# Kernel tuning notes

Measured on AMD Instinct MI355X. Metric: run time of the kernel, lower is better.

Reference implementation:

```python
import jax, jax.numpy as jnp
import numpy as np

H = 1024   # hidden_size
NH = 32    # num_heads
D = H // NH  # head_dim = 32
M = 2      # num_timescales
BMIN, BMAX = 0.85, 0.9995
EPS = 1e-6
ROPE_BASE = 10000.0
LN_EPS = 1e-5


def setup_inputs() -> dict:
    key = jax.random.key(0)
    ks = jax.random.split(key, 8)
    b, t = 4, 1024
    x = jax.random.normal(ks[0], (b, t, H), jnp.float32)
    # xavier-uniform for q/k/v/out (matches _reset_parameters)
    sc = (6.0 / (H + H)) ** 0.5
    Wq = jax.random.uniform(ks[1], (H, H), jnp.float32, -sc, sc)
    Wk = jax.random.uniform(ks[2], (H, H), jnp.float32, -sc, sc)
    Wv = jax.random.uniform(ks[3], (H, H), jnp.float32, -sc, sc)
    Wout = jax.random.uniform(ks[4], (H, H), jnp.float32, -sc, sc)
    bout = jnp.zeros((H,), jnp.float32)
    # beta_proj: random weight, bias set so sigmoid(bias) = linspace(beta_min, beta_max)
    scb = (6.0 / (H + NH * M)) ** 0.5
    Wbeta = jax.random.uniform(ks[5], (NH * M, H), jnp.float32, -scb, scb)
    targets = jnp.linspace(BMIN, BMAX, M)
    bbeta = jnp.tile(jnp.log(targets / (1.0 - targets)), NH)  # repeat 'm -> (h m)'
    # mix_proj initialized to zeros (uniform mixing via softmax)
    Wmix = jnp.zeros((NH * M, H), jnp.float32)
    bmix = jnp.zeros((NH * M,), jnp.float32)
    ln_g = jnp.ones((H,), jnp.float32)
    ln_b = jnp.zeros((H,), jnp.float32)
    return dict(x=x, Wq=Wq, Wk=Wk, Wv=Wv, Wbeta=Wbeta, bbeta=bbeta,
                Wmix=Wmix, bmix=bmix, Wout=Wout, bout=bout, ln_g=ln_g, ln_b=ln_b)


def _rope(u, cos, sin):
    # u: [b,t,h,d] with d even; cos/sin: [1,t,1,d//2]
    half = D // 2
    u1, u2 = u[..., :half], u[..., half:]
    return jnp.concatenate([u1 * cos - u2 * sin, u1 * sin + u2 * cos], axis=-1)


def _forward(x, Wq, Wk, Wv, Wbeta, bbeta, Wmix, bmix, Wout, bout, ln_g, ln_b):
    b, t, _ = x.shape
    q = (x @ Wq.T).reshape(b, t, NH, D)
    k = (x @ Wk.T).reshape(b, t, NH, D)
    v = (x @ Wv.T).reshape(b, t, NH, D)
    # RoPE cache
    half = D // 2
    inv_freq = 1.0 / (ROPE_BASE ** (jnp.arange(half, dtype=jnp.float32) / half))
    freqs = jnp.arange(t, dtype=jnp.float32)[:, None] * inv_freq  # [t,half]
    cos = jnp.cos(freqs)[None, :, None, :]
    sin = jnp.sin(freqs)[None, :, None, :]
    q = _rope(q, cos, sin)
    k = _rope(k, cos, sin)
    phi_q = jax.nn.elu(q) + 1.0
    phi_k = jax.nn.elu(k) + 1.0
    beta = jnp.clip(jax.nn.sigmoid((x @ Wbeta.T + bbeta).reshape(b, t, NH, M)), BMIN, BMAX)
    mix = jax.nn.softmax((x @ Wmix.T + bmix).reshape(b, t, NH, M), axis=-1)

    def step(carry, xs):
        S, K = carry  # S:[b,h,M,d,d]  K:[b,h,M,d]
        pq, pk, vt, bt, mt = xs  # [b,h,d],[b,h,d],[b,h,d],[b,h,M],[b,h,M]
        K = K * bt[..., None] + pk[:, :, None, :]
        S = S * bt[..., None, None] + pk[:, :, None, :, None] * vt[:, :, None, None, :]
        num = jnp.einsum('bhd,bhmdc->bhmc', pq, S)
        den = jnp.einsum('bhd,bhmd->bhm', pq, K) + EPS
        y = jnp.sum(num / den[..., None] * mt[..., None], axis=2)  # [b,h,d]
        return (S, K), y

    S0 = jnp.zeros((b, NH, M, D, D), x.dtype)
    K0 = jnp.zeros((b, NH, M, D), x.dtype)
    tf = lambda a: jnp.moveaxis(a, 1, 0)  # time-major for scan
    _, ys = jax.lax.scan(step, (S0, K0), (tf(phi_q), tf(phi_k), tf(v), tf(beta), tf(mix)))
    y = jnp.moveaxis(ys, 0, 1).reshape(b, t, H) @ Wout.T + bout
    z = x + y  # residual; dropout is identity in eval
    mu = z.mean(-1, keepdims=True)
    var = ((z - mu) ** 2).mean(-1, keepdims=True)
    return (z - mu) / jnp.sqrt(var + LN_EPS) * ln_g + ln_b


def reference(x, Wq, Wk, Wv, Wbeta, bbeta, Wmix, bmix, Wout, bout, ln_g, ln_b):
    return _forward(x, Wq, Wk, Wv, Wbeta, bbeta, Wmix, bmix, Wout, bout, ln_g, ln_b)
```

## Files before the change

kernel.cpp:

```cpp
#include <hip/hip_runtime.h>
#include <math.h>

#define TT 1024
#define BB 4
#define HH 1024
#define NHH 32
#define CL 64
#define NCH (TT/CL)

typedef unsigned short u16;
typedef __attribute__((ext_vector_type(8))) short short8;
typedef __attribute__((ext_vector_type(8))) unsigned short u16x8;
typedef __attribute__((ext_vector_type(4))) float floatx4;

__device__ __forceinline__ float sigmoidf_(float x){ return 1.f/(1.f+expf(-x)); }
__device__ __forceinline__ u16 f2b(float f){
  union { float f; unsigned u; } x; x.f = f;
  unsigned r = x.u + 0x7FFFu + ((x.u >> 16) & 1u);
  return (u16)(r >> 16);
}
__device__ __forceinline__ float b2f(u16 v){
  union { unsigned u; float f; } x; x.u = ((unsigned)v) << 16;
  return x.f;
}

__global__ __launch_bounds__(256) void cast_all_k(
    const float* __restrict__ x, const float* __restrict__ Wq, const float* __restrict__ Wk,
    const float* __restrict__ Wv, const float* __restrict__ Wbeta, const float* __restrict__ Wmix,
    const float* __restrict__ Wout,
    u16* __restrict__ x_bf, u16* __restrict__ Wf, u16* __restrict__ Wout_bf,
    float* __restrict__ ct, float* __restrict__ st)
{
  int gid = blockIdx.x*256 + threadIdx.x;
  if (gid < 16384) {
    int t = gid >> 4, j = gid & 15;
    float invf = powf(10000.f, -(float)j/16.f);
    float ang = (float)t * invf;
    ct[gid] = cosf(ang);
    st[gid] = sinf(ang);
  }
  size_t e = (size_t)gid*4;
  const float* src; u16* dst; size_t so, dof;
  if      (e < 4194304) { src=x;     dst=x_bf;    so=e;          dof=so; }
  else if (e < 5242880) { src=Wq;    dst=Wf;      so=e-4194304;  dof=so; }
  else if (e < 6291456) { src=Wk;    dst=Wf;      so=e-5242880;  dof=so+1048576; }
  else if (e < 7340032) { src=Wv;    dst=Wf;      so=e-6291456;  dof=so+2097152; }
  else if (e < 7405568) { src=Wbeta; dst=Wf;      so=e-7340032;  dof=so+3145728; }
  else if (e < 7471104) { src=Wmix;  dst=Wf;      so=e-7405568;  dof=so+3211264; }
  else                  { src=Wout;  dst=Wout_bf; so=e-7471104;  dof=so; }
  float4 f = *reinterpret_cast<const float4*>(src + so);
  ushort4 u; u.x=f2b(f.x); u.y=f2b(f.y); u.z=f2b(f.z); u.w=f2b(f.w);
  *reinterpret_cast<ushort4*>(dst + dof) = u;
}

__global__ __launch_bounds__(256) void gemm_qkv_k(
    const u16* __restrict__ A, const u16* __restrict__ W,
    const float* __restrict__ ct, const float* __restrict__ st,
    u16* __restrict__ qkv, float* __restrict__ bmraw)
{
  __shared__ u16 As[128*64];
  __shared__ u16 Ws[128*64];
  const int tid = threadIdx.x;
  const int lane = tid & 63;
  const int wave = tid >> 6;
  const int wm = wave >> 1, wn = wave & 1;
  const int bx = blockIdx.x;
  const int row0 = blockIdx.y*128, col0 = bx*128;
  const int lr = lane & 15, lkg = lane >> 4;

  floatx4 acc[4][4];
  #pragma unroll
  for (int mt=0; mt<4; ++mt)
    #pragma unroll
    for (int nt=0; nt<4; ++nt)
      acc[mt][nt] = (floatx4){0.f,0.f,0.f,0.f};

  for (int k0 = 0; k0 < 1024; k0 += 64) {
    __syncthreads();
    #pragma unroll
    for (int it = 0; it < 4; ++it) {
      int li  = it*256 + tid;
      int row = li >> 3, ckp = li & 7;
      int ck  = ckp ^ (row & 7);
      const u16* ga = A + (size_t)(row0+row)*1024 + k0 + ck*8;
      const u16* gw = W + (size_t)(col0+row)*1024 + k0 + ck*8;
      __builtin_amdgcn_global_load_lds(
          (const __attribute__((address_space(1))) void*)ga,
          (__attribute__((address_space(3))) void*)(As + (size_t)(li & ~63)*8), 16, 0, 0);
      __builtin_amdgcn_global_load_lds(
          (const __attribute__((address_space(1))) void*)gw,
          (__attribute__((address_space(3))) void*)(Ws + (size_t)(li & ~63)*8), 16, 0, 0);
    }
    __syncthreads();
    #pragma unroll
    for (int kk = 0; kk < 64; kk += 32) {
      short8 af[4], wf[4];
      const int ckw = (kk >> 3) + lkg;
      #pragma unroll
      for (int t = 0; t < 4; ++t) {
        int rowA = wm*64 + t*16 + lr;
        int rowW = wn*64 + t*16 + lr;
        af[t] = *reinterpret_cast<const short8*>(As + rowA*64 + (ckw ^ (rowA & 7))*8);
        wf[t] = *reinterpret_cast<const short8*>(Ws + rowW*64 + (ckw ^ (rowW & 7))*8);
      }
      #pragma unroll
      for (int mt = 0; mt < 4; ++mt)
        #pragma unroll
        for (int nt = 0; nt < 4; ++nt)
          acc[mt][nt] = __builtin_amdgcn_mfma_f32_16x16x32_bf16(af[mt], wf[nt], acc[mt][nt], 0, 0, 0);
    }
  }
  if (bx < 16) {
    #pragma unroll
    for (int mt = 0; mt < 4; ++mt) {
      #pragma unroll
      for (int r = 0; r < 4; ++r) {
        int row = row0 + wm*64 + mt*16 + lkg*4 + r;
        int t = row & (TT-1);
        float c_ = ct[t*16 + lr], s_ = st[t*16 + lr];
        #pragma unroll
        for (int nt = 0; nt < 4; nt += 2) {
          float u1 = acc[mt][nt][r], u2 = acc[mt][nt+1][r];
          float r1 = u1*c_ - u2*s_;
          float r2 = u1*s_ + u2*c_;
          r1 = r1 > 0.f ? r1+1.f : expf(r1);
          r2 = r2 > 0.f ? r2+1.f : expf(r2);
          int col = col0 + wn*64 + nt*16 + lr;
          qkv[(size_t)row*3072 + col]      = f2b(r1);
          qkv[(size_t)row*3072 + col + 16] = f2b(r2);
        }
      }
    }
  } else if (bx < 24) {
    #pragma unroll
    for (int mt = 0; mt < 4; ++mt)
      #pragma unroll
      for (int r = 0; r < 4; ++r) {
        int row = row0 + wm*64 + mt*16 + lkg*4 + r;
        #pragma unroll
        for (int nt = 0; nt < 4; ++nt) {
          int col = col0 + wn*64 + nt*16 + lr;
          qkv[(size_t)row*3072 + col] = f2b(acc[mt][nt][r]);
        }
      }
  } else {
    #pragma unroll
    for (int mt = 0; mt < 4; ++mt)
      #pragma unroll
      for (int r = 0; r < 4; ++r) {
        int row = row0 + wm*64 + mt*16 + lkg*4 + r;
        #pragma unroll
        for (int nt = 0; nt < 4; ++nt) {
          int col = col0 + wn*64 + nt*16 + lr - 3072;
          bmraw[(size_t)row*128 + col] = acc[mt][nt][r];
        }
      }
  }
}

__global__ __launch_bounds__(256) void gemm_out_k(
    const u16* __restrict__ A, const u16* __restrict__ W,
    const float* __restrict__ xr, const float* __restrict__ bout,
    float* __restrict__ Z)
{
  __shared__ u16 As[128*64];
  __shared__ u16 Ws[64*64];
  const int tid = threadIdx.x;
  const int lane = tid & 63;
  const int wave = tid >> 6;
  const int row0 = blockIdx.y*128, col0 = blockIdx.x*64;
  const int lr = lane & 15, lkg = lane >> 4;
  floatx4 acc[2][4];
  #pragma unroll
  for (int mt=0; mt<2; ++mt)
    #pragma unroll
    for (int nt=0; nt<4; ++nt)
      acc[mt][nt] = (floatx4){0.f,0.f,0.f,0.f};
  for (int k0 = 0; k0 < 1024; k0 += 64) {
    __syncthreads();
    #pragma unroll
    for (int it = 0; it < 4; ++it) {
      int li  = it*256 + tid;
      int row = li >> 3, ckp = li & 7;
      int ck  = ckp ^ (row & 7);
      const u16* ga = A + (size_t)(row0+row)*1024 + k0 + ck*8;
      __builtin_amdgcn_global_load_lds(
          (const __attribute__((address_space(1))) void*)ga,
          (__attribute__((address_space(3))) void*)(As + (size_t)(li & ~63)*8), 16, 0, 0);
    }
    #pragma unroll
    for (int it = 0; it < 2; ++it) {
      int li  = it*256 + tid;
      int row = li >> 3, ckp = li & 7;
      int ck  = ckp ^ (row & 7);
      const u16* gw = W + (size_t)(col0+row)*1024 + k0 + ck*8;
      __builtin_amdgcn_global_load_lds(
          (const __attribute__((address_space(1))) void*)gw,
          (__attribute__((address_space(3))) void*)(Ws + (size_t)(li & ~63)*8), 16, 0, 0);
    }
    __syncthreads();
    #pragma unroll
    for (int kk = 0; kk < 64; kk += 32) {
      short8 af[2], wf[4];
      const int ckw = (kk >> 3) + lkg;
      #pragma unroll
      for (int t = 0; t < 2; ++t) {
        int rowA = wave*32 + t*16 + lr;
        af[t] = *reinterpret_cast<const short8*>(As + rowA*64 + (ckw ^ (rowA & 7))*8);
      }
      #pragma unroll
      for (int t = 0; t < 4; ++t) {
        int rowW = t*16 + lr;
        wf[t] = *reinterpret_cast<const short8*>(Ws + rowW*64 + (ckw ^ (rowW & 7))*8);
      }
      #pragma unroll
      for (int mt = 0; mt < 2; ++mt)
        #pragma unroll
        for (int nt = 0; nt < 4; ++nt)
          acc[mt][nt] = __builtin_amdgcn_mfma_f32_16x16x32_bf16(af[mt], wf[nt], acc[mt][nt], 0, 0, 0);
    }
  }
  #pragma unroll
  for (int mt = 0; mt < 2; ++mt)
    #pragma unroll
    for (int r = 0; r < 4; ++r) {
      int row = row0 + wave*32 + mt*16 + lkg*4 + r;
      #pragma unroll
      for (int nt = 0; nt < 4; ++nt) {
        int col = col0 + nt*16 + lr;
        Z[(size_t)row*HH + col] = acc[mt][nt][r] + bout[col] + xr[(size_t)row*HH + col];
      }
    }
}

__global__ __launch_bounds__(256) void scan_delta_k(
    const u16* __restrict__ qkv, const float* __restrict__ bmraw,
    const float* __restrict__ bbeta,
    float* __restrict__ dS, float* __restrict__ dK,
    float* __restrict__ pLg, float* __restrict__ pg)
{
  __shared__ __align__(16) u16 K2T[2][32][72];
  __shared__ __align__(16) u16 VT[32][72];
  __shared__ float bets[2][64], pbuf[2][64], wjs[2][64], pLs[2];
  const int ch = blockIdx.x, h = blockIdx.y, b = blockIdx.z;
  const int bh = b*NHH + h;
  const int tid = threadIdx.x;
  const int t0 = ch*CL;
  const int j = tid >> 2, oct = tid & 3;
  size_t rowbase = (size_t)(b*TT + t0 + j)*3072 + h*32 + oct*8;
  u16x8 k8 = *reinterpret_cast<const u16x8*>(qkv + rowbase + 1024);
  u16x8 v8 = *reinterpret_cast<const u16x8*>(qkv + rowbase + 2048);
  if (tid < 128) {
    int m = tid & 1, tl = tid >> 1;
    float bv = bmraw[(size_t)(b*TT + t0 + tl)*128 + h*2 + m] + bbeta[h*2 + m];
    bets[m][tl] = fminf(fmaxf(sigmoidf_(bv), 0.85f), 0.9995f);
  }
  #pragma unroll
  for (int dd = 0; dd < 8; ++dd) VT[oct*8+dd][j] = v8[dd];
  __syncthreads();
  if (tid < 128) {
    int m = tid >> 6, l = tid & 63;
    float p = bets[m][l];
    #pragma unroll
    for (int off = 1; off < 64; off <<= 1) {
      float o = __shfl_up(p, off);
      if (l >= off) p *= o;
    }
    pbuf[m][l] = p;
    if (l == 63) pLs[m] = p;
  }
  __syncthreads();
  if (tid < 128) {
    int m = tid >> 6, l = tid & 63;
    wjs[m][l] = pLs[m] / pbuf[m][l];
    pg[(((size_t)bh*NCH + ch)*2 + m)*64 + l] = pbuf[m][l];
  }
  if (tid < 2) pLg[((size_t)bh*NCH + ch)*2 + tid] = pLs[tid];
  __syncthreads();
  float w0 = wjs[0][j], w1 = wjs[1][j];
  #pragma unroll
  for (int dd = 0; dd < 8; ++dd) {
    float kv = b2f(k8[dd]);
    K2T[0][oct*8+dd][j] = f2b(kv*w0);
    K2T[1][oct*8+dd][j] = f2b(kv*w1);
  }
  __syncthreads();
  {
    const int wv = tid >> 6, lane = tid & 63, lr = lane & 15, kg = lane >> 4;
    const int m = wv >> 1, mt = wv & 1;
    floatx4 a0 = (floatx4){0.f,0.f,0.f,0.f}, a1 = (floatx4){0.f,0.f,0.f,0.f};
    #pragma unroll
    for (int ks = 0; ks < 2; ++ks) {
      short8 af = *reinterpret_cast<const short8*>(&K2T[m][mt*16 + lr][ks*32 + kg*8]);
      short8 b0 = *reinterpret_cast<const short8*>(&VT[lr][ks*32 + kg*8]);
      short8 b1 = *reinterpret_cast<const short8*>(&VT[16 + lr][ks*32 + kg*8]);
      a0 = __builtin_amdgcn_mfma_f32_16x16x32_bf16(af, b0, a0, 0, 0, 0);
      a1 = __builtin_amdgcn_mfma_f32_16x16x32_bf16(af, b1, a1, 0, 0, 0);
    }
    size_t base = (((size_t)bh*NCH + ch)*2 + m)*1024;
    #pragma unroll
    for (int r = 0; r < 4; ++r) {
      int d = mt*16 + kg*4 + r;
      dS[base + d*32 + lr]      = a0[r];
      dS[base + d*32 + 16 + lr] = a1[r];
    }
  }
  if (tid < 64) {
    int m = tid >> 5, d = tid & 31;
    float s = 0.f;
    #pragma unroll
    for (int g = 0; g < 8; ++g) {
      u16x8 kk = *reinterpret_cast<const u16x8*>(&K2T[m][d][g*8]);
      #pragma unroll
      for (int dd = 0; dd < 8; ++dd) s += b2f(kk[dd]);
    }
    dK[(((size_t)bh*NCH + ch)*2 + m)*32 + d] = s;
  }
}

__global__ __launch_bounds__(256) void scan_state_k(
    float* dSS0, float* dKK0, const float* __restrict__ pLg)
{
  const int bhm = blockIdx.x >> 2, part = blockIdx.x & 3;
  const int bh = bhm >> 1, m = bhm & 1;
  const int idx = part*256 + threadIdx.x;
  float pls[NCH], dv[NCH];
  #pragma unroll
  for (int ch = 0; ch < NCH; ++ch) pls[ch] = pLg[((size_t)bh*NCH + ch)*2 + m];
  #pragma unroll
  for (int ch = 0; ch < NCH; ++ch) dv[ch] = dSS0[(((size_t)bh*NCH + ch)*2 + m)*1024 + idx];
  float S = 0.f;
  #pragma unroll
  for (int ch = 0; ch < NCH; ++ch) {
    dSS0[(((size_t)bh*NCH + ch)*2 + m)*1024 + idx] = S;
    S = fmaf(pls[ch], S, dv[ch]);
  }
  if (part == 0 && threadIdx.x < 32) {
    int d = threadIdx.x;
    float kv[NCH];
    #pragma unroll
    for (int ch = 0; ch < NCH; ++ch) kv[ch] = dKK0[(((size_t)bh*NCH + ch)*2 + m)*32 + d];
    float K0 = 0.f;
    #pragma unroll
    for (int ch = 0; ch < NCH; ++ch) {
      dKK0[(((size_t)bh*NCH + ch)*2 + m)*32 + d] = K0;
      K0 = fmaf(pls[ch], K0, kv[ch]);
    }
  }
}

__global__ __launch_bounds__(256) void scan_apply_k(
    const u16* __restrict__ qkv, const float* __restrict__ bmraw,
    const float* __restrict__ bmix,
    const float* __restrict__ S0g, const float* __restrict__ K0g,
    const float* __restrict__ pg, u16* __restrict__ yb)
{
  __shared__ __align__(16) u16 Qs[64][32], Ks[64][32];
  __shared__ __align__(16) u16 VT[32][72];
  __shared__ __align__(16) u16 At[2][64][72];
  __shared__ __align__(16) u16 S0T[2][2][32][40];
  __shared__ float K0s[2][32];
  __shared__ float pbv[2][64], ipb[2][64], mixs[2][64], coef[2][64];
  const int ch = blockIdx.x, h = blockIdx.y, b = blockIdx.z;
  const int bh = b*NHH + h;
  const int tid = threadIdx.x;
  const int t0 = ch*CL;
  {
    int j = tid >> 2, oct = tid & 3;
    size_t rb = (size_t)(b*TT + t0 + j)*3072 + h*32 + oct*8;
    u16x8 q8 = *reinterpret_cast<const u16x8*>(qkv + rb);
    u16x8 k8 = *reinterpret_cast<const u16x8*>(qkv + rb + 1024);
    u16x8 v8 = *reinterpret_cast<const u16x8*>(qkv + rb + 2048);
    *reinterpret_cast<u16x8*>(&Qs[j][oct*8]) = q8;
    *reinterpret_cast<u16x8*>(&Ks[j][oct*8]) = k8;
    #pragma unroll
    for (int dd = 0; dd < 8; ++dd) VT[oct*8+dd][j] = v8[dd];
  }
  for (int u = tid; u < 2048; u += 256) {
    int m = u >> 10, r = u & 1023, d = r >> 5, c = r & 31;
    float val = S0g[(((size_t)bh*NCH + ch)*2 + m)*1024 + r];
    u16 hv = f2b(val);
    float lo = val - b2f(hv);
    S0T[m][0][c][d] = hv;
    S0T[m][1][c][d] = f2b(lo);
  }
  if (tid < 64) {
    int m = tid >> 5, d = tid & 31;
    K0s[m][d] = K0g[(((size_t)bh*NCH + ch)*2 + m)*32 + d];
  }
  if (tid < 128) {
    int m = tid & 1, i = tid >> 1;
    float p = pg[(((size_t)bh*NCH + ch)*2 + m)*64 + i];
    pbv[m][i] = p;
    ipb[m][i] = 1.f/p;
  } else if (tid < 192) {
    int i = tid - 128;
    size_t rb = (size_t)(b*TT + t0 + i)*128 + 64 + h*2;
    float a0 = bmraw[rb]   + bmix[h*2];
    float a1 = bmraw[rb+1] + bmix[h*2+1];
    float mx = fmaxf(a0, a1);
    float e0 = expf(a0-mx), e1 = expf(a1-mx);
    float inv = 1.f/(e0+e1);
    mixs[0][i] = e0*inv; mixs[1][i] = e1*inv;
  }
  __syncthreads();
  {
    const int wv = tid >> 6, lane = tid & 63, lr = lane & 15, kg = lane >> 4;
    short8 aq = *reinterpret_cast<const short8*>(&Qs[wv*16 + lr][kg*8]);
    #pragma unroll
    for (int nt = 0; nt < 4; ++nt) {
      short8 bk = *reinterpret_cast<const short8*>(&Ks[nt*16 + lr][kg*8]);
      floatx4 a0 = (floatx4){0.f,0.f,0.f,0.f};
      a0 = __builtin_amdgcn_mfma_f32_16x16x32_bf16(aq, bk, a0, 0, 0, 0);
      int jg = nt*16 + lr;
      float ip0 = ipb[0][jg], ip1 = ipb[1][jg];
      #pragma unroll
      for (int r = 0; r < 4; ++r) {
        int ig = wv*16 + kg*4 + r;
        float val = a0[r];
        bool ok = (jg <= ig);
        At[0][ig][jg] = f2b(ok ? val*ip0 : 0.f);
        At[1][ig][jg] = f2b(ok ? val*ip1 : 0.f);
      }
    }
  }
  __syncthreads();
  if (tid < 128) {
    int m = tid & 1, i = tid >> 1;
    float qK0 = 0.f;
    #pragma unroll
    for (int g = 0; g < 4; ++g) {
      u16x8 qq = *reinterpret_cast<const u16x8*>(&Qs[i][g*8]);
      #pragma unroll
      for (int dd = 0; dd < 8; ++dd) qK0 = fmaf(b2f(qq[dd]), K0s[m][g*8+dd], qK0);
    }
    float As_ = 0.f;
    #pragma unroll
    for (int g = 0; g < 8; ++g) {
      u16x8 aa = *reinterpret_cast<const u16x8*>(&At[m][i][g*8]);
      #pragma unroll
      for (int dd = 0; dd < 8; ++dd) As_ += b2f(aa[dd]);
    }
    float den = pbv[m][i]*(qK0 + As_) + 1e-6f;
    coef[m][i] = mixs[m][i]*pbv[m][i]/den;
  }
  __syncthreads();
  {
    const int wv = tid >> 6, lane = tid & 63, lr = lane & 15, kg = lane >> 4;
    const int i0 = wv*16;
    floatx4 accY[2][2];
    #pragma unroll
    for (int m = 0; m < 2; ++m)
      #pragma unroll
      for (int nt = 0; nt < 2; ++nt)
        accY[m][nt] = (floatx4){0.f,0.f,0.f,0.f};
    short8 aq = *reinterpret_cast<const short8*>(&Qs[i0 + lr][kg*8]);
    #pragma unroll
    for (int m = 0; m < 2; ++m)
      #pragma unroll
      for (int nt = 0; nt < 2; ++nt) {
        short8 bhi = *reinterpret_cast<const short8*>(&S0T[m][0][nt*16 + lr][kg*8]);
        short8 blo = *reinterpret_cast<const short8*>(&S0T[m][1][nt*16 + lr][kg*8]);
        accY[m][nt] = __builtin_amdgcn_mfma_f32_16x16x32_bf16(aq, bhi, accY[m][nt], 0, 0, 0);
        accY[m][nt] = __builtin_amdgcn_mfma_f32_16x16x32_bf16(aq, blo, accY[m][nt], 0, 0, 0);
      }
    #pragma unroll
    for (int ks = 0; ks < 2; ++ks) {
      short8 a0f = *reinterpret_cast<const short8*>(&At[0][i0 + lr][ks*32 + kg*8]);
      short8 a1f = *reinterpret_cast<const short8*>(&At[1][i0 + lr][ks*32 + kg*8]);
      short8 b0 = *reinterpret_cast<const short8*>(&VT[lr][ks*32 + kg*8]);
      short8 b1 = *reinterpret_cast<const short8*>(&VT[16 + lr][ks*32 + kg*8]);
      accY[0][0] = __builtin_amdgcn_mfma_f32_16x16x32_bf16(a0f, b0, accY[0][0], 0, 0, 0);
      accY[0][1] = __builtin_amdgcn_mfma_f32_16x16x32_bf16(a0f, b1, accY[0][1], 0, 0, 0);
      accY[1][0] = __builtin_amdgcn_mfma_f32_16x16x32_bf16(a1f, b0, accY[1][0], 0, 0, 0);
      accY[1][1] = __builtin_amdgcn_mfma_f32_16x16x32_bf16(a1f, b1, accY[1][1], 0, 0, 0);
    }
    #pragma unroll
    for (int r = 0; r < 4; ++r) {
      int i = i0 + kg*4 + r;
      float c0 = coef[0][i], c1 = coef[1][i];
      size_t ob = (size_t)(b*TT + t0 + i)*HH + h*32;
      yb[ob + lr]      = f2b(c0*accY[0][0][r] + c1*accY[1][0][r]);
      yb[ob + 16 + lr] = f2b(c0*accY[0][1][r] + c1*accY[1][1][r]);
    }
  }
}

__global__ __launch_bounds__(256) void ln_k(
    const float* __restrict__ z, const float* __restrict__ g,
    const float* __restrict__ bta, float* __restrict__ out)
{
  const int row = blockIdx.x;
  const int tid = threadIdx.x;
  size_t o = (size_t)row*HH/4 + tid;
  float4 zv = reinterpret_cast<const float4*>(z)[o];
  float sum = zv.x+zv.y+zv.z+zv.w;
  float sq  = zv.x*zv.x + zv.y*zv.y + zv.z*zv.z + zv.w*zv.w;
  #pragma unroll
  for (int off=1; off<64; off<<=1){ sum += __shfl_xor(sum, off); sq += __shfl_xor(sq, off); }
  __shared__ float s1[4], s2[4];
  int w = tid>>6;
  if ((tid&63)==0){ s1[w]=sum; s2[w]=sq; }
  __syncthreads();
  sum = s1[0]+s1[1]+s1[2]+s1[3];
  sq  = s2[0]+s2[1]+s2[2]+s2[3];
  float mu  = sum * (1.f/1024.f);
  float var = sq * (1.f/1024.f) - mu*mu;
  float rstd = rsqrtf(var + 1e-5f);
  float4 gv = reinterpret_cast<const float4*>(g)[tid];
  float4 bv = reinterpret_cast<const float4*>(bta)[tid];
  float4 ov;
  ov.x = (zv.x-mu)*rstd*gv.x + bv.x;
  ov.y = (zv.y-mu)*rstd*gv.y + bv.y;
  ov.z = (zv.z-mu)*rstd*gv.z + bv.z;
  ov.w = (zv.w-mu)*rstd*gv.w + bv.w;
  reinterpret_cast<float4*>(out)[o] = ov;
}

extern "C" void kernel_launch(void* const* d_in, const int* in_sizes, int n_in,
                              void* d_out, int out_size, void* d_ws, size_t ws_size,
                              hipStream_t stream)
{
  const float* x     = (const float*)d_in[0];
  const float* Wq    = (const float*)d_in[1];
  const float* Wk    = (const float*)d_in[2];
  const float* Wv    = (const float*)d_in[3];
  const float* Wbeta = (const float*)d_in[4];
  const float* bbeta = (const float*)d_in[5];
  const float* Wmix  = (const float*)d_in[6];
  const float* bmix  = (const float*)d_in[7];
  const float* Wout  = (const float*)d_in[8];
  const float* bout  = (const float*)d_in[9];
  const float* ln_g  = (const float*)d_in[10];
  const float* ln_b  = (const float*)d_in[11];
  float* out = (float*)d_out;

  float* ws = (float*)d_ws;
  float* ct      = ws;
  float* st      = ws + 16384;
  u16*   x_bf    = (u16*)(ws + 32768);
  u16*   Wf      = (u16*)(ws + 2129920);
  u16*   Wout_bf = (u16*)(ws + 3768320);
  u16*   qkv     = (u16*)(ws + 4292608);
  float* bmraw   = ws + 10584064;
  float* dSS0    = ws + 11108352;
  float* dKK0    = ws + 15302656;
  float* pLg     = ws + 15433728;
  float* pg      = ws + 15437824;
  u16*   y_bf    = x_bf;
  float* z       = dSS0;

  cast_all_k<<<8320, 256, 0, stream>>>(x, Wq, Wk, Wv, Wbeta, Wmix, Wout,
                                       x_bf, Wf, Wout_bf, ct, st);
  gemm_qkv_k<<<dim3(25, 32), 256, 0, stream>>>(x_bf, Wf, ct, st, qkv, bmraw);
  dim3 gscan(NCH, 32, 4);
  scan_delta_k<<<gscan, 256, 0, stream>>>(qkv, bmraw, bbeta, dSS0, dKK0, pLg, pg);
  scan_state_k<<<1024, 256, 0, stream>>>(dSS0, dKK0, pLg);
  scan_apply_k<<<gscan, 256, 0, stream>>>(qkv, bmraw, bmix, dSS0, dKK0, pg, y_bf);
  gemm_out_k<<<dim3(16, 32), 256, 0, stream>>>(y_bf, Wout_bf, x, bout, z);
  ln_k<<<4096, 256, 0, stream>>>(z, ln_g, ln_b, out);
}
```

Baseline: 210.2 us.

## Fuse chunked scan into one sequential-chunk kernel with on-chip state

Replaces the three-kernel chunked scan (per-chunk deltas, cross-chunk state prefix, apply) with a single kernel. Each block owns one (batch, head, half of value dims) and walks all chunks sequentially, keeping the running S and K state in shared memory and prefetching the next chunk's q/k/v and gate inputs into registers. This removes the global round trips for dS/dK/pLg/pg and two launches. In exchange the grid shrinks to 256 blocks that each run a 16-step serial loop, so parallelism drops, and the QK^T and K-side work is duplicated across the two value halves.

```diff
diff --git a/kernel.cpp b/kernel.cpp
--- a/kernel.cpp
+++ b/kernel.cpp
@@ -233,255 +233,210 @@
     }
 }
 
-__global__ __launch_bounds__(256) void scan_delta_k(
+__global__ __launch_bounds__(256) void scan_fused_k(
     const u16* __restrict__ qkv, const float* __restrict__ bmraw,
-    const float* __restrict__ bbeta,
-    float* __restrict__ dS, float* __restrict__ dK,
-    float* __restrict__ pLg, float* __restrict__ pg)
+    const float* __restrict__ bbeta, const float* __restrict__ bmix,
+    u16* __restrict__ yb)
 {
+  __shared__ __align__(16) u16 Qs[64][40], Ks[64][40];
+  __shared__ __align__(16) u16 VT[16][72];
   __shared__ __align__(16) u16 K2T[2][32][72];
-  __shared__ __align__(16) u16 VT[32][72];
-  __shared__ float bets[2][64], pbuf[2][64], wjs[2][64], pLs[2];
-  const int ch = blockIdx.x, h = blockIdx.y, b = blockIdx.z;
-  const int bh = b*NHH + h;
+  __shared__ __align__(16) u16 At[2][64][72];
+  __shared__ __align__(16) u16 S0T[2][2][16][40];
+  __shared__ float Ss[2][32][17];
+  __shared__ float K0s[2][32];
+  __shared__ float bets[2][64], pbv[2][64], ipb[2][64], wjs[2][64], mixs[2][64], coef[2][64];
+  __shared__ float pLs[2];
+
+  const int chalf = blockIdx.x, h = blockIdx.y, b = blockIdx.z;
   const int tid = threadIdx.x;
-  const int t0 = ch*CL;
-  const int j = tid >> 2, oct = tid & 3;
-  size_t rowbase = (size_t)(b*TT + t0 + j)*3072 + h*32 + oct*8;
-  u16x8 k8 = *reinterpret_cast<const u16x8*>(qkv + rowbase + 1024);
-  u16x8 v8 = *reinterpret_cast<const u16x8*>(qkv + rowbase + 2048);
-  if (tid < 128) {
-    int m = tid & 1, tl = tid >> 1;
-    float bv = bmraw[(size_t)(b*TT + t0 + tl)*128 + h*2 + m] + bbeta[h*2 + m];
-    bets[m][tl] = fminf(fmaxf(sigmoidf_(bv), 0.85f), 0.9995f);
+  const int lane = tid & 63, wv = tid >> 6;
+  const int lr = lane & 15, kg = lane >> 4;
+  const int jrow = tid >> 2, oct = tid & 3;
+
+  for (int u = tid; u < 2*32*17; u += 256) ((float*)Ss)[u] = 0.f;
+  if (tid < 64) K0s[tid>>5][tid&31] = 0.f;
+
+  const float bb  = (tid < 128) ? bbeta[h*2 + (tid&1)] : 0.f;
+  const float bm0 = bmix[h*2], bm1 = bmix[h*2+1];
+
+  u16x8 q8, k8; ushort4 v4; float bmv = 0.f, mr0 = 0.f, mr1 = 0.f;
+  {
+    size_t rb = (size_t)(b*TT + jrow)*3072 + h*32;
+    q8 = *reinterpret_cast<const u16x8*>(qkv + rb + oct*8);
+    k8 = *reinterpret_cast<const u16x8*>(qkv + rb + 1024 + oct*8);
+    v4 = *reinterpret_cast<const ushort4*>(qkv + rb + 2048 + chalf*16 + oct*4);
+    if (tid < 128) bmv = bmraw[(size_t)(b*TT + (tid>>1))*128 + h*2 + (tid&1)];
+    else if (tid < 192) {
+      int i = tid - 128;
+      size_t mb = (size_t)(b*TT + i)*128 + 64 + h*2;
+      mr0 = bmraw[mb]; mr1 = bmraw[mb+1];
+    }
   }
-  #pragma unroll
-  for (int dd = 0; dd < 8; ++dd) VT[oct*8+dd][j] = v8[dd];
-  __syncthreads();
-  if (tid < 128) {
-    int m = tid >> 6, l = tid & 63;
-    float p = bets[m][l];
-    #pragma unroll
-    for (int off = 1; off < 64; off <<= 1) {
-      float o = __shfl_up(p, off);
-      if (l >= off) p *= o;
-    }
-    pbuf[m][l] = p;
-    if (l == 63) pLs[m] = p;
-  }
-  __syncthreads();
-  if (tid < 128) {
-    int m = tid >> 6, l = tid & 63;
-    wjs[m][l] = pLs[m] / pbuf[m][l];
-    pg[(((size_t)bh*NCH + ch)*2 + m)*64 + l] = pbuf[m][l];
-  }
-  if (tid < 2) pLg[((size_t)bh*NCH + ch)*2 + tid] = pLs[tid];
-  __syncthreads();
-  float w0 = wjs[0][j], w1 = wjs[1][j];
-  #pragma unroll
-  for (int dd = 0; dd < 8; ++dd) {
-    float kv = b2f(k8[dd]);
-    K2T[0][oct*8+dd][j] = f2b(kv*w0);
-    K2T[1][oct*8+dd][j] = f2b(kv*w1);
-  }
-  __syncthreads();
-  {
-    const int wv = tid >> 6, lane = tid & 63, lr = lane & 15, kg = lane >> 4;
-    const int m = wv >> 1, mt = wv & 1;
-    floatx4 a0 = (floatx4){0.f,0.f,0.f,0.f}, a1 = (floatx4){0.f,0.f,0.f,0.f};
-    #pragma unroll
-    for (int ks = 0; ks < 2; ++ks) {
-      short8 af = *reinterpret_cast<const short8*>(&K2T[m][mt*16 + lr][ks*32 + kg*8]);
-      short8 b0 = *reinterpret_cast<const short8*>(&VT[lr][ks*32 + kg*8]);
-      short8 b1 = *reinterpret_cast<const short8*>(&VT[16 + lr][ks*32 + kg*8]);
-      a0 = __builtin_amdgcn_mfma_f32_16x16x32_bf16(af, b0, a0, 0, 0, 0);
-      a1 = __builtin_amdgcn_mfma_f32_16x16x32_bf16(af, b1, a1, 0, 0, 0);
-    }
-    size_t base = (((size_t)bh*NCH + ch)*2 + m)*1024;
-    #pragma unroll
-    for (int r = 0; r < 4; ++r) {
-      int d = mt*16 + kg*4 + r;
-      dS[base + d*32 + lr]      = a0[r];
-      dS[base + d*32 + 16 + lr] = a1[r];
-    }
-  }
-  if (tid < 64) {
-    int m = tid >> 5, d = tid & 31;
-    float s = 0.f;
-    #pragma unroll
-    for (int g = 0; g < 8; ++g) {
-      u16x8 kk = *reinterpret_cast<const u16x8*>(&K2T[m][d][g*8]);
-      #pragma unroll
-      for (int dd = 0; dd < 8; ++dd) s += b2f(kk[dd]);
-    }
-    dK[(((size_t)bh*NCH + ch)*2 + m)*32 + d] = s;
-  }
-}
-
-__global__ __launch_bounds__(256) void scan_state_k(
-    float* dSS0, float* dKK0, const float* __restrict__ pLg)
-{
-  const int bhm = blockIdx.x >> 2, part = blockIdx.x & 3;
-  const int bh = bhm >> 1, m = bhm & 1;
-  const int idx = part*256 + threadIdx.x;
-  float pls[NCH], dv[NCH];
-  #pragma unroll
-  for (int ch = 0; ch < NCH; ++ch) pls[ch] = pLg[((size_t)bh*NCH + ch)*2 + m];
-  #pragma unroll
-  for (int ch = 0; ch < NCH; ++ch) dv[ch] = dSS0[(((size_t)bh*NCH + ch)*2 + m)*1024 + idx];
-  float S = 0.f;
-  #pragma unroll
+
   for (int ch = 0; ch < NCH; ++ch) {
-    dSS0[(((size_t)bh*NCH + ch)*2 + m)*1024 + idx] = S;
-    S = fmaf(pls[ch], S, dv[ch]);
-  }
-  if (part == 0 && threadIdx.x < 32) {
-    int d = threadIdx.x;
-    float kv[NCH];
-    #pragma unroll
-    for (int ch = 0; ch < NCH; ++ch) kv[ch] = dKK0[(((size_t)bh*NCH + ch)*2 + m)*32 + d];
-    float K0 = 0.f;
-    #pragma unroll
-    for (int ch = 0; ch < NCH; ++ch) {
-      dKK0[(((size_t)bh*NCH + ch)*2 + m)*32 + d] = K0;
-      K0 = fmaf(pls[ch], K0, kv[ch]);
-    }
-  }
-}
-
-__global__ __launch_bounds__(256) void scan_apply_k(
-    const u16* __restrict__ qkv, const float* __restrict__ bmraw,
-    const float* __restrict__ bmix,
-    const float* __restrict__ S0g, const float* __restrict__ K0g,
-    const float* __restrict__ pg, u16* __restrict__ yb)
-{
-  __shared__ __align__(16) u16 Qs[64][32], Ks[64][32];
-  __shared__ __align__(16) u16 VT[32][72];
-  __shared__ __align__(16) u16 At[2][64][72];
-  __shared__ __align__(16) u16 S0T[2][2][32][40];
-  __shared__ float K0s[2][32];
-  __shared__ float pbv[2][64], ipb[2][64], mixs[2][64], coef[2][64];
-  const int ch = blockIdx.x, h = blockIdx.y, b = blockIdx.z;
-  const int bh = b*NHH + h;
-  const int tid = threadIdx.x;
-  const int t0 = ch*CL;
-  {
-    int j = tid >> 2, oct = tid & 3;
-    size_t rb = (size_t)(b*TT + t0 + j)*3072 + h*32 + oct*8;
-    u16x8 q8 = *reinterpret_cast<const u16x8*>(qkv + rb);
-    u16x8 k8 = *reinterpret_cast<const u16x8*>(qkv + rb + 1024);
-    u16x8 v8 = *reinterpret_cast<const u16x8*>(qkv + rb + 2048);
-    *reinterpret_cast<u16x8*>(&Qs[j][oct*8]) = q8;
-    *reinterpret_cast<u16x8*>(&Ks[j][oct*8]) = k8;
-    #pragma unroll
-    for (int dd = 0; dd < 8; ++dd) VT[oct*8+dd][j] = v8[dd];
-  }
-  for (int u = tid; u < 2048; u += 256) {
-    int m = u >> 10, r = u & 1023, d = r >> 5, c = r & 31;
-    float val = S0g[(((size_t)bh*NCH + ch)*2 + m)*1024 + r];
-    u16 hv = f2b(val);
-    float lo = val - b2f(hv);
-    S0T[m][0][c][d] = hv;
-    S0T[m][1][c][d] = f2b(lo);
-  }
-  if (tid < 64) {
-    int m = tid >> 5, d = tid & 31;
-    K0s[m][d] = K0g[(((size_t)bh*NCH + ch)*2 + m)*32 + d];
-  }
-  if (tid < 128) {
-    int m = tid & 1, i = tid >> 1;
-    float p = pg[(((size_t)bh*NCH + ch)*2 + m)*64 + i];
-    pbv[m][i] = p;
-    ipb[m][i] = 1.f/p;
-  } else if (tid < 192) {
-    int i = tid - 128;
-    size_t rb = (size_t)(b*TT + t0 + i)*128 + 64 + h*2;
-    float a0 = bmraw[rb]   + bmix[h*2];
-    float a1 = bmraw[rb+1] + bmix[h*2+1];
-    float mx = fmaxf(a0, a1);
-    float e0 = expf(a0-mx), e1 = expf(a1-mx);
-    float inv = 1.f/(e0+e1);
-    mixs[0][i] = e0*inv; mixs[1][i] = e1*inv;
-  }
-  __syncthreads();
-  {
-    const int wv = tid >> 6, lane = tid & 63, lr = lane & 15, kg = lane >> 4;
-    short8 aq = *reinterpret_cast<const short8*>(&Qs[wv*16 + lr][kg*8]);
+    const int t0 = ch*CL;
+    __syncthreads();
+    *reinterpret_cast<u16x8*>(&Qs[jrow][oct*8]) = q8;
+    *reinterpret_cast<u16x8*>(&Ks[jrow][oct*8]) = k8;
+    u16x8 k8c = k8;
+    {
+      const u16* vp = reinterpret_cast<const u16*>(&v4);
+      #pragma unroll
+      for (int u2 = 0; u2 < 4; ++u2) VT[oct*4+u2][jrow] = vp[u2];
+    }
+    float mr0c = mr0, mr1c = mr1;
+    if (tid < 128) bets[tid&1][tid>>1] = fminf(fmaxf(sigmoidf_(bmv + bb), 0.85f), 0.9995f);
+    if (ch < NCH-1) {
+      int t0n = t0 + CL;
+      size_t rb = (size_t)(b*TT + t0n + jrow)*3072 + h*32;
+      q8 = *reinterpret_cast<const u16x8*>(qkv + rb + oct*8);
+      k8 = *reinterpret_cast<const u16x8*>(qkv + rb + 1024 + oct*8);
+      v4 = *reinterpret_cast<const ushort4*>(qkv + rb + 2048 + chalf*16 + oct*4);
+      if (tid < 128) bmv = bmraw[(size_t)(b*TT + t0n + (tid>>1))*128 + h*2 + (tid&1)];
+      else if (tid < 192) {
+        int i = tid - 128;
+        size_t mb = (size_t)(b*TT + t0n + i)*128 + 64 + h*2;
+        mr0 = bmraw[mb]; mr1 = bmraw[mb+1];
+      }
+    }
+    __syncthreads();
+    if (tid < 128) {
+      float p = bets[wv][lane];
+      #pragma unroll
+      for (int off = 1; off < 64; off <<= 1) {
+        float o = __shfl_up(p, off);
+        if (lane >= off) p *= o;
+      }
+      float pl = __shfl(p, 63);
+      pbv[wv][lane] = p;
+      ipb[wv][lane] = 1.f/p;
+      wjs[wv][lane] = pl/p;
+      if (lane == 63) pLs[wv] = p;
+    } else if (tid < 192) {
+      int i = tid - 128;
+      float a0v = mr0c + bm0, a1v = mr1c + bm1;
+      float mx = fmaxf(a0v, a1v);
+      float e0 = expf(a0v-mx), e1 = expf(a1v-mx);
+      float inv = 1.f/(e0+e1);
+      mixs[0][i] = e0*inv; mixs[1][i] = e1*inv;
+    }
+    floatx4 a0r[4];
+    {
+      short8 aq = *reinterpret_cast<const short8*>(&Qs[wv*16 + lr][kg*8]);
+      #pragma unroll
+      for (int nt = 0; nt < 4; ++nt) {
+        short8 bk = *reinterpret_cast<const short8*>(&Ks[nt*16 + lr][kg*8]);
+        a0r[nt] = (floatx4){0.f,0.f,0.f,0.f};
+        a0r[nt] = __builtin_amdgcn_mfma_f32_16x16x32_bf16(aq, bk, a0r[nt], 0, 0, 0);
+      }
+    }
+    #pragma unroll
+    for (int i2 = 0; i2 < 4; ++i2) {
+      int e = tid*4 + i2;
+      int m = e >> 9, rem = e & 511, c = rem >> 5, d = rem & 31;
+      float val = Ss[m][d][c];
+      u16 hv = f2b(val);
+      S0T[m][0][c][d] = hv;
+      S0T[m][1][c][d] = f2b(val - b2f(hv));
+    }
+    __syncthreads();
     #pragma unroll
     for (int nt = 0; nt < 4; ++nt) {
-      short8 bk = *reinterpret_cast<const short8*>(&Ks[nt*16 + lr][kg*8]);
-      floatx4 a0 = (floatx4){0.f,0.f,0.f,0.f};
-      a0 = __builtin_amdgcn_mfma_f32_16x16x32_bf16(aq, bk, a0, 0, 0, 0);
       int jg = nt*16 + lr;
       float ip0 = ipb[0][jg], ip1 = ipb[1][jg];
       #pragma unroll
       for (int r = 0; r < 4; ++r) {
         int ig = wv*16 + kg*4 + r;
-        float val = a0[r];
+        float val = a0r[nt][r];
         bool ok = (jg <= ig);
         At[0][ig][jg] = f2b(ok ? val*ip0 : 0.f);
         At[1][ig][jg] = f2b(ok ? val*ip1 : 0.f);
       }
     }
-  }
-  __syncthreads();
-  if (tid < 128) {
-    int m = tid & 1, i = tid >> 1;
-    float qK0 = 0.f;
-    #pragma unroll
-    for (int g = 0; g < 4; ++g) {
-      u16x8 qq = *reinterpret_cast<const u16x8*>(&Qs[i][g*8]);
-      #pragma unroll
-      for (int dd = 0; dd < 8; ++dd) qK0 = fmaf(b2f(qq[dd]), K0s[m][g*8+dd], qK0);
-    }
-    float As_ = 0.f;
-    #pragma unroll
-    for (int g = 0; g < 8; ++g) {
-      u16x8 aa = *reinterpret_cast<const u16x8*>(&At[m][i][g*8]);
-      #pragma unroll
-      for (int dd = 0; dd < 8; ++dd) As_ += b2f(aa[dd]);
-    }
-    float den = pbv[m][i]*(qK0 + As_) + 1e-6f;
-    coef[m][i] = mixs[m][i]*pbv[m][i]/den;
-  }
-  __syncthreads();
-  {
-    const int wv = tid >> 6, lane = tid & 63, lr = lane & 15, kg = lane >> 4;
-    const int i0 = wv*16;
-    floatx4 accY[2][2];
-    #pragma unroll
-    for (int m = 0; m < 2; ++m)
-      #pragma unroll
-      for (int nt = 0; nt < 2; ++nt)
-        accY[m][nt] = (floatx4){0.f,0.f,0.f,0.f};
-    short8 aq = *reinterpret_cast<const short8*>(&Qs[i0 + lr][kg*8]);
-    #pragma unroll
-    for (int m = 0; m < 2; ++m)
-      #pragma unroll
-      for (int nt = 0; nt < 2; ++nt) {
-        short8 bhi = *reinterpret_cast<const short8*>(&S0T[m][0][nt*16 + lr][kg*8]);
-        short8 blo = *reinterpret_cast<const short8*>(&S0T[m][1][nt*16 + lr][kg*8]);
-        accY[m][nt] = __builtin_amdgcn_mfma_f32_16x16x32_bf16(aq, bhi, accY[m][nt], 0, 0, 0);
-        accY[m][nt] = __builtin_amdgcn_mfma_f32_16x16x32_bf16(aq, blo, accY[m][nt], 0, 0, 0);
-      }
-    #pragma unroll
-    for (int ks = 0; ks < 2; ++ks) {
-      short8 a0f = *reinterpret_cast<const short8*>(&At[0][i0 + lr][ks*32 + kg*8]);
-      short8 a1f = *reinterpret_cast<const short8*>(&At[1][i0 + lr][ks*32 + kg*8]);
-      short8 b0 = *reinterpret_cast<const short8*>(&VT[lr][ks*32 + kg*8]);
-      short8 b1 = *reinterpret_cast<const short8*>(&VT[16 + lr][ks*32 + kg*8]);
-      accY[0][0] = __builtin_amdgcn_mfma_f32_16x16x32_bf16(a0f, b0, accY[0][0], 0, 0, 0);
-      accY[0][1] = __builtin_amdgcn_mfma_f32_16x16x32_bf16(a0f, b1, accY[0][1], 0, 0, 0);
-      accY[1][0] = __builtin_amdgcn_mfma_f32_16x16x32_bf16(a1f, b0, accY[1][0], 0, 0, 0);
-      accY[1][1] = __builtin_amdgcn_mfma_f32_16x16x32_bf16(a1f, b1, accY[1][1], 0, 0, 0);
-    }
-    #pragma unroll
-    for (int r = 0; r < 4; ++r) {
-      int i = i0 + kg*4 + r;
-      float c0 = coef[0][i], c1 = coef[1][i];
-      size_t ob = (size_t)(b*TT + t0 + i)*HH + h*32;
-      yb[ob + lr]      = f2b(c0*accY[0][0][r] + c1*accY[1][0][r]);
-      yb[ob + 16 + lr] = f2b(c0*accY[0][1][r] + c1*accY[1][1][r]);
+    {
+      float w0 = wjs[0][jrow], w1 = wjs[1][jrow];
+      #pragma unroll
+      for (int dd = 0; dd < 8; ++dd) {
+        float kv = b2f(k8c[dd]);
+        K2T[0][oct*8+dd][jrow] = f2b(kv*w0);
+        K2T[1][oct*8+dd][jrow] = f2b(kv*w1);
+      }
+    }
+    __syncthreads();
+    if (tid < 128) {
+      int m = tid & 1, i = tid >> 1;
+      float qK0 = 0.f;
+      #pragma unroll
+      for (int g = 0; g < 4; ++g) {
+        u16x8 qq = *reinterpret_cast<const u16x8*>(&Qs[i][g*8]);
+        #pragma unroll
+        for (int dd = 0; dd < 8; ++dd) qK0 = fmaf(b2f(qq[dd]), K0s[m][g*8+dd], qK0);
+      }
+      float As_ = 0.f;
+      #pragma unroll
+      for (int g = 0; g < 8; ++g) {
+        u16x8 aa = *reinterpret_cast<const u16x8*>(&At[m][i][g*8]);
+        #pragma unroll
+        for (int dd = 0; dd < 8; ++dd) As_ += b2f(aa[dd]);
+      }
+      float den = pbv[m][i]*(qK0 + As_) + 1e-6f;
+      coef[m][i] = mixs[m][i]*pbv[m][i]/den;
+    } else {
+      int m = wv - 2;
+      float pl = pLs[m];
+      #pragma unroll
+      for (int dt = 0; dt < 2; ++dt) {
+        floatx4 acc = (floatx4){0.f,0.f,0.f,0.f};
+        #pragma unroll
+        for (int ks = 0; ks < 2; ++ks) {
+          short8 af = *reinterpret_cast<const short8*>(&K2T[m][dt*16 + lr][ks*32 + kg*8]);
+          short8 bv = *reinterpret_cast<const short8*>(&VT[lr][ks*32 + kg*8]);
+          acc = __builtin_amdgcn_mfma_f32_16x16x32_bf16(af, bv, acc, 0, 0, 0);
+        }
+        #pragma unroll
+        for (int r = 0; r < 4; ++r) {
+          int d = dt*16 + kg*4 + r;
+          Ss[m][d][lr] = fmaf(pl, Ss[m][d][lr], acc[r]);
+        }
+      }
+    }
+    __syncthreads();
+    {
+      floatx4 accY[2];
+      short8 aq = *reinterpret_cast<const short8*>(&Qs[wv*16 + lr][kg*8]);
+      #pragma unroll
+      for (int m = 0; m < 2; ++m) {
+        accY[m] = (floatx4){0.f,0.f,0.f,0.f};
+        short8 bhi = *reinterpret_cast<const short8*>(&S0T[m][0][lr][kg*8]);
+        short8 blo = *reinterpret_cast<const short8*>(&S0T[m][1][lr][kg*8]);
+        accY[m] = __builtin_amdgcn_mfma_f32_16x16x32_bf16(aq, bhi, accY[m], 0, 0, 0);
+        accY[m] = __builtin_amdgcn_mfma_f32_16x16x32_bf16(aq, blo, accY[m], 0, 0, 0);
+        #pragma unroll
+        for (int ks = 0; ks < 2; ++ks) {
+          short8 af = *reinterpret_cast<const short8*>(&At[m][wv*16 + lr][ks*32 + kg*8]);
+          short8 bv = *reinterpret_cast<const short8*>(&VT[lr][ks*32 + kg*8]);
+          accY[m] = __builtin_amdgcn_mfma_f32_16x16x32_bf16(af, bv, accY[m], 0, 0, 0);
+        }
+      }
+      #pragma unroll
+      for (int r = 0; r < 4; ++r) {
+        int i = wv*16 + kg*4 + r;
+        float c0 = coef[0][i], c1 = coef[1][i];
+        yb[(size_t)(b*TT + t0 + i)*HH + h*32 + chalf*16 + lr]
+            = f2b(c0*accY[0][r] + c1*accY[1][r]);
+      }
+    }
+    if (tid < 64) {
+      int m = tid >> 5, d = tid & 31;
+      float s = 0.f;
+      #pragma unroll
+      for (int g = 0; g < 8; ++g) {
+        u16x8 kk = *reinterpret_cast<const u16x8*>(&K2T[m][d][g*8]);
+        #pragma unroll
+        for (int dd = 0; dd < 8; ++dd) s += b2f(kk[dd]);
+      }
+      K0s[m][d] = fmaf(pLs[m], K0s[m][d], s);
     }
   }
 }
@@ -543,20 +498,13 @@
   u16*   Wout_bf = (u16*)(ws + 3768320);
   u16*   qkv     = (u16*)(ws + 4292608);
   float* bmraw   = ws + 10584064;
-  float* dSS0    = ws + 11108352;
-  float* dKK0    = ws + 15302656;
-  float* pLg     = ws + 15433728;
-  float* pg      = ws + 15437824;
+  float* z       = ws + 11108352;
   u16*   y_bf    = x_bf;
-  float* z       = dSS0;
 
   cast_all_k<<<8320, 256, 0, stream>>>(x, Wq, Wk, Wv, Wbeta, Wmix, Wout,
                                        x_bf, Wf, Wout_bf, ct, st);
   gemm_qkv_k<<<dim3(25, 32), 256, 0, stream>>>(x_bf, Wf, ct, st, qkv, bmraw);
-  dim3 gscan(NCH, 32, 4);
-  scan_delta_k<<<gscan, 256, 0, stream>>>(qkv, bmraw, bbeta, dSS0, dKK0, pLg, pg);
-  scan_state_k<<<1024, 256, 0, stream>>>(dSS0, dKK0, pLg);
-  scan_apply_k<<<gscan, 256, 0, stream>>>(qkv, bmraw, bmix, dSS0, dKK0, pg, y_bf);
+  scan_fused_k<<<dim3(2, 32, 4), 256, 0, stream>>>(qkv, bmraw, bbeta, bmix, y_bf);
   gemm_out_k<<<dim3(16, 32), 256, 0, stream>>>(y_bf, Wout_bf, x, bout, z);
   ln_k<<<4096, 256, 0, stream>>>(z, ln_g, ln_b, out);
 }
```

After: 233.6 us. 11.1% more time.
